# Performance work log

Measured on AMD Instinct MI355X. Metric: run time of the kernel, lower is better.

## Reference

```python
import math
import jax, jax.numpy as jnp
import numpy as np

N = 256  # size (power of 2)
B = 512  # batch
STEEPNESS = 10.0  # cauchy distribution steepness


def _bitonic_network(n):
    # n must be a power of 2; every layer then has exactly n//2 compare-exchanges.
    num_blocks = int(math.log2(n))
    sa_l, sb_l, cmin_l, cmax_l = [], [], [], []
    for block_idx in range(num_blocks):
        for layer_idx in range(block_idx + 1):
            m = 2 ** (block_idx - layer_idx)
            split_a = np.zeros((n // 2, n), np.float32)
            split_b = np.zeros((n // 2, n), np.float32)
            combine_min = np.zeros((n, n // 2), np.float32)
            combine_max = np.zeros((n, n // 2), np.float32)
            count = 0
            for i in range(0, n, 2 * m):
                for j in range(m):
                    ix = i + j
                    a, b = ix, ix + m
                    split_a[count, a] = 1.0
                    split_b[count, b] = 1.0
                    if (ix // 2 ** (block_idx + 1)) % 2 == 1:
                        a, b = b, a
                    combine_min[a, count] = 1.0
                    combine_max[b, count] = 1.0
                    count += 1
            sa_l.append(split_a); sb_l.append(split_b)
            cmin_l.append(combine_min); cmax_l.append(combine_max)
    return (np.stack(sa_l), np.stack(sb_l), np.stack(cmin_l), np.stack(cmax_l))


def setup_inputs() -> dict:
    key = jax.random.key(0)
    vectors = jax.random.normal(key, (B, N), dtype=jnp.float32)
    sa, sb, cmin, cmax = _bitonic_network(N)
    return {
        "vectors": vectors,
        "split_a": jnp.asarray(sa),       # [L, n/2, n]
        "split_b": jnp.asarray(sb),       # [L, n/2, n]
        "combine_min": jnp.asarray(cmin), # [L, n, n/2]
        "combine_max": jnp.asarray(cmax), # [L, n, n/2]
    }


def reference(vectors, split_a, split_b, combine_min, combine_max):
    # Faithful to the given source: x (=vectors) is never updated inside the
    # loop; only the soft permutation matrix X is accumulated and returned.
    Bsz, n = vectors.shape
    X0 = jnp.broadcast_to(jnp.eye(n, dtype=vectors.dtype), (Bsz, n, n))

    def step(X, mats):
        sa, sb, cmin, cmax = mats
        a = vectors @ sa.T  # [B, k]
        b = vectors @ sb.T  # [B, k]
        # cauchy interpolation
        alpha = jnp.arctan(STEEPNESS * (b - a)) / jnp.pi + 0.5  # [B, k]
        aX = jnp.einsum('bij,kj->bik', X, sa)  # [B, n, k]
        bX = jnp.einsum('bij,kj->bik', X, sb)  # [B, n, k]
        al = alpha[:, None, :]
        w_min = al * aX + (1.0 - al) * bX
        w_max = (1.0 - al) * aX + al * bX
        X_new = jnp.einsum('bik,jk->bij', w_max, cmax) + jnp.einsum('bik,jk->bij', w_min, cmin)
        return X_new, None

    X, _ = jax.lax.scan(step, X0, (split_a, split_b, combine_min, combine_max))
    return X
```

## Files before the change

### kernel.cpp

```cpp
#include <hip/hip_runtime.h>
#include <math.h>

typedef float vf4 __attribute__((ext_vector_type(4)));

static constexpr int LLB[36] = {
  0,
  1,0,
  2,1,0,
  3,2,1,0,
  4,3,2,1,0,
  5,4,3,2,1,0,
  6,5,4,3,2,1,0,
  7,6,5,4,3,2,1,0
};
static constexpr int LBLK[36] = {
  0,
  1,1,
  2,2,2,
  3,3,3,3,
  4,4,4,4,4,
  5,5,5,5,5,5,
  6,6,6,6,6,6,6,
  7,7,7,7,7,7,7,7
};

__global__ __launch_bounds__(128) void k_ugen(const float* __restrict__ vec,
                                              float* __restrict__ U) {
  const int b = blockIdx.x;
  const int k = threadIdx.x;
  const float* v = vec + b * 256;
  float* ub = U + (size_t)b * 4608;
  #pragma unroll
  for (int l = 0; l < 36; ++l) {
    const int lb  = LLB[l];
    const int blk = LBLK[l];
    const int m = 1 << lb;
    const int p = ((k >> lb) << (lb + 1)) | (k & (m - 1));
    const int q = p + m;
    const int d = (p >> (blk + 1)) & 1;
    const float alpha =
        atanf(10.0f * (v[q] - v[p])) * 0.3183098861837907f + 0.5f;
    ub[l * 128 + k] = d ? (1.0f - alpha) : alpha;
  }
}

__global__ __launch_bounds__(256) void k_phase1(const float* __restrict__ U,
                                                float* __restrict__ staged) {
  const int b = blockIdx.x;
  const int i = threadIdx.x;
  const int g = i >> 6;
  const int il = i & 63;
  float r[64];
  #pragma unroll
  for (int j = 0; j < 64; ++j) r[j] = (j == il) ? 1.0f : 0.0f;

  const int ubase = __builtin_amdgcn_readfirstlane(b * 4608 + 32 * g);
  #pragma unroll
  for (int l = 0; l < 21; ++l) {
    const int lb = LLB[l];
    const int m = 1 << lb;
    const float* ul = U + ubase + l * 128;
    #pragma unroll
    for (int kl = 0; kl < 32; ++kl) {
      const int p = ((kl >> lb) << (lb + 1)) | (kl & (m - 1));
      const int q = p + m;
      const float u = ul[kl];
      const float t  = r[p] - r[q];
      const float np = fmaf(u, t, r[q]);
      const float nq = fmaf(-u, t, r[p]);
      r[p] = np;
      r[q] = nq;
    }
  }
  float* op = staged + ((size_t)b * 256 + i) * 64;
  #pragma unroll
  for (int t = 0; t < 16; ++t)
    *(float4*)(op + 4 * t) =
        make_float4(r[4*t], r[4*t+1], r[4*t+2], r[4*t+3]);
}

__global__ __launch_bounds__(256) void k_phase23(const float* __restrict__ U,
                                                 const float* __restrict__ staged,
                                                 float* __restrict__ out) {
  const int bg = blockIdx.x;
  const int b = bg >> 2;
  const int g = bg & 3;
  const int c  = threadIdx.x >> 6;
  const int rr = threadIdx.x & 63;
  const int i = g * 64 + rr;
  __shared__ float4 ex4[4096];
  float y[64];

  const int ub = __builtin_amdgcn_readfirstlane(b * 4608);

  {
    const int ap = g >> 1;
    if ((c >> 1) == ap) {
      const float* u21 = U + ub + 21 * 128 + 64 * ap;
      const bool sm = ((c & 1) == (g & 1));
      const float* srp = staged + ((size_t)b * 256 + i) * 64;
      #pragma unroll
      for (int t = 0; t < 16; ++t) {
        const float4 s4 = *(const float4*)(srp + 4 * t);
        const float u0 = u21[4*t+0], u1 = u21[4*t+1];
        const float u2 = u21[4*t+2], u3 = u21[4*t+3];
        y[4*t+0] = s4.x * (sm ? u0 : 1.0f - u0);
        y[4*t+1] = s4.y * (sm ? u1 : 1.0f - u1);
        y[4*t+2] = s4.z * (sm ? u2 : 1.0f - u2);
        y[4*t+3] = s4.w * (sm ? u3 : 1.0f - u3);
      }
    } else {
      #pragma unroll
      for (int j = 0; j < 64; ++j) y[j] = 0.0f;
    }
  }

  const int cb = __builtin_amdgcn_readfirstlane(32 * c);

  #pragma unroll
  for (int l = 22; l < 28; ++l) {
    const int lb = LLB[l];
    const int m = 1 << lb;
    const float* ul = U + ub + l * 128 + cb;
    #pragma unroll
    for (int kl = 0; kl < 32; ++kl) {
      const int p = ((kl >> lb) << (lb + 1)) | (kl & (m - 1));
      const int q = p + m;
      const float u = ul[kl];
      const float t  = y[p] - y[q];
      const float np = fmaf(u, t, y[q]);
      const float nq = fmaf(-u, t, y[p]);
      y[p] = np;
      y[q] = nq;
    }
  }

  #pragma unroll
  for (int t = 0; t < 16; ++t)
    ex4[(c * 16 + t) * 64 + rr] =
        make_float4(y[4*t], y[4*t+1], y[4*t+2], y[4*t+3]);
  __syncthreads();
  {
    const int pc = c ^ 2;
    const float* u28 = U + ub + 28 * 128 + 64 * (c & 1);
    #pragma unroll
    for (int t = 0; t < 16; ++t) {
      const float4 p4 = ex4[(pc * 16 + t) * 64 + rr];
      const float u0 = u28[4*t+0], u1 = u28[4*t+1];
      const float u2 = u28[4*t+2], u3 = u28[4*t+3];
      y[4*t+0] = fmaf(u0, y[4*t+0] - p4.x, p4.x);
      y[4*t+1] = fmaf(u1, y[4*t+1] - p4.y, p4.y);
      y[4*t+2] = fmaf(u2, y[4*t+2] - p4.z, p4.z);
      y[4*t+3] = fmaf(u3, y[4*t+3] - p4.w, p4.w);
    }
  }
  __syncthreads();

  #pragma unroll
  for (int t = 0; t < 16; ++t)
    ex4[(c * 16 + t) * 64 + rr] =
        make_float4(y[4*t], y[4*t+1], y[4*t+2], y[4*t+3]);
  __syncthreads();
  {
    const int pc = c ^ 1;
    const float* u29 = U + ub + 29 * 128 + 64 * (c >> 1);
    #pragma unroll
    for (int t = 0; t < 16; ++t) {
      const float4 p4 = ex4[(pc * 16 + t) * 64 + rr];
      const float u0 = u29[4*t+0], u1 = u29[4*t+1];
      const float u2 = u29[4*t+2], u3 = u29[4*t+3];
      y[4*t+0] = fmaf(u0, y[4*t+0] - p4.x, p4.x);
      y[4*t+1] = fmaf(u1, y[4*t+1] - p4.y, p4.y);
      y[4*t+2] = fmaf(u2, y[4*t+2] - p4.z, p4.z);
      y[4*t+3] = fmaf(u3, y[4*t+3] - p4.w, p4.w);
    }
  }

  #pragma unroll
  for (int l = 30; l < 36; ++l) {
    const int lb = LLB[l];
    const int m = 1 << lb;
    const float* ul = U + ub + l * 128 + cb;
    #pragma unroll
    for (int kl = 0; kl < 32; ++kl) {
      const int p = ((kl >> lb) << (lb + 1)) | (kl & (m - 1));
      const int q = p + m;
      const float u = ul[kl];
      const float t  = y[p] - y[q];
      const float np = fmaf(u, t, y[q]);
      const float nq = fmaf(-u, t, y[p]);
      y[p] = np;
      y[q] = nq;
    }
  }

  __syncthreads();
  #pragma unroll
  for (int t = 0; t < 16; ++t) {
    const int q = c * 16 + t;
    ex4[rr * 64 + (q ^ (rr & 7))] =
        make_float4(y[4*t], y[4*t+1], y[4*t+2], y[4*t+3]);
  }
  __syncthreads();
  {
    float4* out4 = (float4*)out + ((size_t)(b * 256 + g * 64)) * 64;
    const int tid = threadIdx.x;
    #pragma unroll
    for (int it = 0; it < 16; ++it) {
      const int fq = it * 256 + tid;
      const int r = fq >> 6;
      const int q = fq & 63;
      const float4 v4 = ex4[r * 64 + (q ^ (r & 7))];
      __builtin_nontemporal_store(*(const vf4*)&v4, (vf4*)&out4[fq]);
    }
  }
}

extern "C" void kernel_launch(void* const* d_in, const int* in_sizes, int n_in,
                              void* d_out, int out_size, void* d_ws, size_t ws_size,
                              hipStream_t stream) {
  const float* vec = (const float*)d_in[0];
  float* out = (float*)d_out;
  float* U = (float*)d_ws;
  float* staged = U + (size_t)512 * 4608;

  hipLaunchKernelGGL(k_ugen,    dim3(512),  dim3(128), 0, stream, vec, U);
  hipLaunchKernelGGL(k_phase1,  dim3(512),  dim3(256), 0, stream, U, staged);
  hipLaunchKernelGGL(k_phase23, dim3(2048), dim3(256), 0, stream, U, staged, out);
}
```

Measured before the change: 225.4 us.

## Fuse phase-1 butterfly layers into main kernel, dropping staged buffer

Merges the first 21 butterfly layers into the phase-2/3 kernel. Each thread now rebuilds its one-hot row and runs those layers in registers, instead of reading a 64-float row written to a global staging buffer by a separate kernel. This removes one kernel launch and the global write and read of the staged intermediate. In exchange, the phase-1 work is repeated by every one of the four column groups in a block, about four times the original phase-1 arithmetic. Half of those threads then throw their result away.

```diff
diff --git a/kernel.cpp b/kernel.cpp
--- a/kernel.cpp
+++ b/kernel.cpp
@@ -44,70 +44,54 @@
   }
 }
 
-__global__ __launch_bounds__(256) void k_phase1(const float* __restrict__ U,
-                                                float* __restrict__ staged) {
-  const int b = blockIdx.x;
-  const int i = threadIdx.x;
-  const int g = i >> 6;
-  const int il = i & 63;
-  float r[64];
-  #pragma unroll
-  for (int j = 0; j < 64; ++j) r[j] = (j == il) ? 1.0f : 0.0f;
-
-  const int ubase = __builtin_amdgcn_readfirstlane(b * 4608 + 32 * g);
-  #pragma unroll
-  for (int l = 0; l < 21; ++l) {
-    const int lb = LLB[l];
-    const int m = 1 << lb;
-    const float* ul = U + ubase + l * 128;
-    #pragma unroll
-    for (int kl = 0; kl < 32; ++kl) {
-      const int p = ((kl >> lb) << (lb + 1)) | (kl & (m - 1));
-      const int q = p + m;
-      const float u = ul[kl];
-      const float t  = r[p] - r[q];
-      const float np = fmaf(u, t, r[q]);
-      const float nq = fmaf(-u, t, r[p]);
-      r[p] = np;
-      r[q] = nq;
-    }
-  }
-  float* op = staged + ((size_t)b * 256 + i) * 64;
-  #pragma unroll
-  for (int t = 0; t < 16; ++t)
-    *(float4*)(op + 4 * t) =
-        make_float4(r[4*t], r[4*t+1], r[4*t+2], r[4*t+3]);
-}
-
-__global__ __launch_bounds__(256) void k_phase23(const float* __restrict__ U,
-                                                 const float* __restrict__ staged,
-                                                 float* __restrict__ out) {
+__global__ __launch_bounds__(256) void k_main(const float* __restrict__ U,
+                                              float* __restrict__ out) {
   const int bg = blockIdx.x;
   const int b = bg >> 2;
   const int g = bg & 3;
   const int c  = threadIdx.x >> 6;
   const int rr = threadIdx.x & 63;
-  const int i = g * 64 + rr;
   __shared__ float4 ex4[4096];
   float y[64];
 
   const int ub = __builtin_amdgcn_readfirstlane(b * 4608);
 
   {
+    float r[64];
+    #pragma unroll
+    for (int j = 0; j < 64; ++j) r[j] = (j == rr) ? 1.0f : 0.0f;
+
+    const int ubase = __builtin_amdgcn_readfirstlane(b * 4608 + 32 * g);
+    #pragma unroll
+    for (int l = 0; l < 21; ++l) {
+      const int lb = LLB[l];
+      const int m = 1 << lb;
+      const float* ul = U + ubase + l * 128;
+      #pragma unroll
+      for (int kl = 0; kl < 32; ++kl) {
+        const int p = ((kl >> lb) << (lb + 1)) | (kl & (m - 1));
+        const int q = p + m;
+        const float u = ul[kl];
+        const float t  = r[p] - r[q];
+        const float np = fmaf(u, t, r[q]);
+        const float nq = fmaf(-u, t, r[p]);
+        r[p] = np;
+        r[q] = nq;
+      }
+    }
+
     const int ap = g >> 1;
     if ((c >> 1) == ap) {
       const float* u21 = U + ub + 21 * 128 + 64 * ap;
       const bool sm = ((c & 1) == (g & 1));
-      const float* srp = staged + ((size_t)b * 256 + i) * 64;
       #pragma unroll
       for (int t = 0; t < 16; ++t) {
-        const float4 s4 = *(const float4*)(srp + 4 * t);
         const float u0 = u21[4*t+0], u1 = u21[4*t+1];
         const float u2 = u21[4*t+2], u3 = u21[4*t+3];
-        y[4*t+0] = s4.x * (sm ? u0 : 1.0f - u0);
-        y[4*t+1] = s4.y * (sm ? u1 : 1.0f - u1);
-        y[4*t+2] = s4.z * (sm ? u2 : 1.0f - u2);
-        y[4*t+3] = s4.w * (sm ? u3 : 1.0f - u3);
+        y[4*t+0] = r[4*t+0] * (sm ? u0 : 1.0f - u0);
+        y[4*t+1] = r[4*t+1] * (sm ? u1 : 1.0f - u1);
+        y[4*t+2] = r[4*t+2] * (sm ? u2 : 1.0f - u2);
+        y[4*t+3] = r[4*t+3] * (sm ? u3 : 1.0f - u3);
       }
     } else {
       #pragma unroll
@@ -222,9 +206,7 @@
   const float* vec = (const float*)d_in[0];
   float* out = (float*)d_out;
   float* U = (float*)d_ws;
-  float* staged = U + (size_t)512 * 4608;
-
-  hipLaunchKernelGGL(k_ugen,    dim3(512),  dim3(128), 0, stream, vec, U);
-  hipLaunchKernelGGL(k_phase1,  dim3(512),  dim3(256), 0, stream, U, staged);
-  hipLaunchKernelGGL(k_phase23, dim3(2048), dim3(256), 0, stream, U, staged, out);
+
+  hipLaunchKernelGGL(k_ugen, dim3(512),  dim3(128), 0, stream, vec, U);
+  hipLaunchKernelGGL(k_main, dim3(2048), dim3(256), 0, stream, U, out);
 }
```

After: 260.1 us. 15.4% more time.
